# Performance work log

Hardware: AMD Instinct MI355X
Metric: run time of the kernel (lower is better)

Reference implementation:

```python
import jax, jax.numpy as jnp
import numpy as np
import math

B, T, C = 4, 1024, 768
H, K = 12, 10
D = C // H  # 64


def setup_inputs() -> dict:
    key = jax.random.key(0)
    ks = jax.random.split(key, 8)
    s = 1.0 / math.sqrt(C)
    return {
        "hidden_states": jax.random.normal(ks[0], (B, T, C), jnp.float32),
        "ucb_count_score": jax.random.uniform(ks[1], (B, H, T, T), jnp.float32),
        "Wq": jax.random.normal(ks[2], (C, C), jnp.float32) * s,
        "bq": jnp.zeros((C,), jnp.float32),
        "Wk": jax.random.normal(ks[3], (C, C), jnp.float32) * s,
        "bk": jnp.zeros((C,), jnp.float32),
        "Wv": jax.random.normal(ks[4], (C, C), jnp.float32) * s,
        "bv": jnp.zeros((C,), jnp.float32),
        "Wo": jax.random.normal(ks[5], (C, C), jnp.float32) * s,
        "bo": jnp.zeros((C,), jnp.float32),
        "counter": 2000,
        "ucb": 1,
    }


def _heads(x):
    # [B,T,C] -> [B,H,T,D]
    return x.reshape(B, T, H, D).transpose(0, 2, 1, 3)


def reference(hidden_states, ucb_count_score, Wq, bq, Wk, bk, Wv, bv, Wo, bo, counter, ucb):
    q = _heads(hidden_states @ Wq + bq)
    k = _heads(hidden_states @ Wk + bk)
    v = _heads(hidden_states @ Wv + bv)

    scores = jnp.einsum("bhqd,bhkd->bhqk", q, k) / math.sqrt(D)
    att = jax.nn.softmax(scores, axis=-1)

    if ucb and counter >= 1000:  # ucb_activation_step
        log_t = math.log(float(counter))
        ucb_scores = att + 1.0 * jnp.sqrt(log_t / (ucb_count_score + 1e-8))  # ucb_beta=1.0
        _, top_idx = jax.lax.top_k(ucb_scores, K)  # [B,H,T,K]
        # scatter 1.0 at top-k positions along last axis
        flat_idx = top_idx.reshape(-1, K)            # [N,K], N=B*H*T
        n = flat_idx.shape[0]
        mask = jnp.zeros((n, T), att.dtype).at[jnp.arange(n)[:, None], flat_idx].set(1.0)
        mask = mask.reshape(B, H, T, T)
        updated_count = ucb_count_score + mask
        sel = att * mask
        attention_probs = sel / (sel.sum(axis=-1, keepdims=True) + 1e-8)
    else:
        attention_probs = att
        updated_count = ucb_count_score

    ctx = jnp.einsum("bhqk,bhkd->bhqd", attention_probs, v)
    ctx = ctx.transpose(0, 2, 1, 3).reshape(B, T, C)
    out = ctx @ Wo + bo  # proj_dropout is identity in eval
    return out, attention_probs, updated_count
```

## Files before the change

kernel.cpp:

```cpp
#include <hip/hip_runtime.h>
#include <math.h>

namespace {

constexpr int Bc = 4, Tc = 1024, Cch = 768, Hc = 12, Dc = 64, KSEL = 10;
constexpr size_t BTC    = (size_t)Bc * Tc * Cch;
constexpr size_t PROBSN = (size_t)Bc * Hc * Tc * Tc;
constexpr size_t CC     = (size_t)Cch * Cch;

typedef __attribute__((ext_vector_type(8))) short          bf16x8;
typedef __attribute__((ext_vector_type(4))) float          f32x4;
typedef __attribute__((ext_vector_type(4))) unsigned short u16x4;
typedef __attribute__((ext_vector_type(8))) unsigned short u16x8;

__device__ __forceinline__ unsigned short bf16rne(float x) {
  unsigned int u = __float_as_uint(x);
  return (unsigned short)((u + 0x7FFFu + ((u >> 16) & 1u)) >> 16);
}
__device__ __forceinline__ float bf16tof(unsigned short h) {
  return __uint_as_float(((unsigned int)h) << 16);
}

template <int CTRL, int RM, bool BC>
__device__ __forceinline__ float dppmovf(float x, float oldv) {
  return __int_as_float(__builtin_amdgcn_update_dpp(
      __float_as_int(oldv), __float_as_int(x), CTRL, RM, 0xf, BC));
}

__device__ __forceinline__ float wave_fmax(float x) {
  x = fmaxf(x, dppmovf<0x111, 0xf, false>(x, x));
  x = fmaxf(x, dppmovf<0x112, 0xf, false>(x, x));
  x = fmaxf(x, dppmovf<0x114, 0xf, false>(x, x));
  x = fmaxf(x, dppmovf<0x118, 0xf, false>(x, x));
  x = fmaxf(x, dppmovf<0x142, 0xa, false>(x, x));
  x = fmaxf(x, dppmovf<0x143, 0xc, false>(x, x));
  return __int_as_float(__builtin_amdgcn_readlane(__float_as_int(x), 63));
}

__device__ __forceinline__ float wave_fsum(float x) {
  x += dppmovf<0x111, 0xf, true>(x, 0.f);
  x += dppmovf<0x112, 0xf, true>(x, 0.f);
  x += dppmovf<0x114, 0xf, true>(x, 0.f);
  x += dppmovf<0x118, 0xf, true>(x, 0.f);
  x += dppmovf<0x142, 0xa, true>(x, 0.f);
  x += dppmovf<0x143, 0xc, true>(x, 0.f);
  return __int_as_float(__builtin_amdgcn_readlane(__float_as_int(x), 63));
}

template <int CTRL, int RM>
__device__ __forceinline__ unsigned long long dppmax64_step(unsigned long long k) {
  const int lo = (int)(unsigned)(k & 0xFFFFFFFFull);
  const int hi = (int)(unsigned)(k >> 32);
  const int lo2 = __builtin_amdgcn_update_dpp(lo, lo, CTRL, RM, 0xf, false);
  const int hi2 = __builtin_amdgcn_update_dpp(hi, hi, CTRL, RM, 0xf, false);
  const unsigned long long k2 =
      ((unsigned long long)(unsigned)hi2 << 32) | (unsigned)lo2;
  return (k2 > k) ? k2 : k;
}

__device__ __forceinline__ unsigned long long wave_kmax(unsigned long long k) {
  k = dppmax64_step<0x111, 0xf>(k);
  k = dppmax64_step<0x112, 0xf>(k);
  k = dppmax64_step<0x114, 0xf>(k);
  k = dppmax64_step<0x118, 0xf>(k);
  k = dppmax64_step<0x142, 0xa>(k);
  k = dppmax64_step<0x143, 0xc>(k);
  const int lo = __builtin_amdgcn_readlane((int)(unsigned)(k & 0xFFFFFFFFull), 63);
  const int hi = __builtin_amdgcn_readlane((int)(unsigned)(k >> 32), 63);
  return ((unsigned long long)(unsigned)hi << 32) | (unsigned)lo;
}

__global__ __launch_bounds__(256) void split_plane(
    const float* __restrict__ src,
    unsigned short* __restrict__ h, unsigned short* __restrict__ l)
{
  const size_t i = (size_t)(blockIdx.x * 256 + threadIdx.x) * 4;
  const float4 v = *(const float4*)&src[i];
  const float xs[4] = {v.x, v.y, v.z, v.w};
  u16x4 hh, ll;
  #pragma unroll
  for (int e = 0; e < 4; ++e) {
    const unsigned short hb = bf16rne(xs[e]);
    hh[e] = hb;
    ll[e] = bf16rne(xs[e] - bf16tof(hb));
  }
  *(u16x4*)&h[i] = hh;
  *(u16x4*)&l[i] = ll;
}

__global__ __launch_bounds__(256) void splitT_w(
    const float* __restrict__ W,
    unsigned short* __restrict__ th, unsigned short* __restrict__ tl)
{
  __shared__ float tile[32][33];
  const int n0 = blockIdx.x * 32, k0 = blockIdx.y * 32;
  const int x = threadIdx.x & 31, y = threadIdx.x >> 5;

  #pragma unroll
  for (int i = 0; i < 4; ++i) {
    const int kk = y * 4 + i;
    tile[kk][x] = W[(size_t)(k0 + kk) * Cch + n0 + x];
  }
  __syncthreads();
  #pragma unroll
  for (int i = 0; i < 4; ++i) {
    const int nn = y * 4 + i;
    const float v = tile[x][nn];
    const unsigned short hb = bf16rne(v);
    th[(size_t)(n0 + nn) * Cch + k0 + x] = hb;
    tl[(size_t)(n0 + nn) * Cch + k0 + x] = bf16rne(v - bf16tof(hb));
  }
}

__global__ __launch_bounds__(256) void qkv_mfma(
    const unsigned short* __restrict__ hidh, const unsigned short* __restrict__ hidl,
    const unsigned short* __restrict__ wqth, const unsigned short* __restrict__ wqtl,
    const unsigned short* __restrict__ wkth, const unsigned short* __restrict__ wktl,
    const unsigned short* __restrict__ wvth, const unsigned short* __restrict__ wvtl,
    const float* __restrict__ bq, const float* __restrict__ bk,
    const float* __restrict__ bv,
    unsigned short* __restrict__ qh, unsigned short* __restrict__ ql,
    unsigned short* __restrict__ kh, unsigned short* __restrict__ kl,
    float* __restrict__ V)
{
  const int z = blockIdx.z;
  const unsigned short* __restrict__ Bhp = (z == 0) ? wqth : (z == 1) ? wkth : wvth;
  const unsigned short* __restrict__ Blp = (z == 0) ? wqtl : (z == 1) ? wktl : wvtl;
  const float* __restrict__ bias = (z == 0) ? bq : (z == 1) ? bk : bv;

  const int m0 = blockIdx.y * 64;
  const int n0 = blockIdx.x * 128;

  __shared__ unsigned short Ah[64][72],  Al[64][72];
  __shared__ unsigned short Bh[128][72], Bl[128][72];

  const int t    = threadIdx.x;
  const int lane = t & 63;
  const int wv   = t >> 6;
  const int wq   = (wv >> 1) * 32;
  const int wk   = (wv & 1) * 64;
  const int fr   = lane & 15;
  const int fg   = lane >> 4;

  f32x4 acc[2][4] = {};

  for (int k0 = 0; k0 < Cch; k0 += 64) {
    __syncthreads();
    #pragma unroll
    for (int i = 0; i < 2; ++i) {
      const int id = t + 256*i;
      const int r = id >> 3, c8 = (id & 7) * 8;
      *(u16x8*)&Ah[r][c8] = *(const u16x8*)&hidh[(size_t)(m0 + r)*Cch + k0 + c8];
      *(u16x8*)&Al[r][c8] = *(const u16x8*)&hidl[(size_t)(m0 + r)*Cch + k0 + c8];
    }
    #pragma unroll
    for (int i = 0; i < 4; ++i) {
      const int id = t + 256*i;
      const int r = id >> 3, c8 = (id & 7) * 8;
      *(u16x8*)&Bh[r][c8] = *(const u16x8*)&Bhp[(size_t)(n0 + r)*Cch + k0 + c8];
      *(u16x8*)&Bl[r][c8] = *(const u16x8*)&Blp[(size_t)(n0 + r)*Cch + k0 + c8];
    }
    __syncthreads();

    #pragma unroll
    for (int g2 = 0; g2 < 2; ++g2) {
      const int dof = g2*32 + 8*fg;
      bf16x8 aH[2], aL[2];
      #pragma unroll
      for (int qt = 0; qt < 2; ++qt) {
        aH[qt] = *(const bf16x8*)&Ah[wq + qt*16 + fr][dof];
        aL[qt] = *(const bf16x8*)&Al[wq + qt*16 + fr][dof];
      }
      #pragma unroll
      for (int kt = 0; kt < 4; ++kt) {
        const bf16x8 bH = *(const bf16x8*)&Bh[wk + kt*16 + fr][dof];
        const bf16x8 bL = *(const bf16x8*)&Bl[wk + kt*16 + fr][dof];
        #pragma unroll
        for (int qt = 0; qt < 2; ++qt) {
          acc[qt][kt] = __builtin_amdgcn_mfma_f32_16x16x32_bf16(
              aH[qt], bH, acc[qt][kt], 0, 0, 0);
          acc[qt][kt] = __builtin_amdgcn_mfma_f32_16x16x32_bf16(
              aH[qt], bL, acc[qt][kt], 0, 0, 0);
          acc[qt][kt] = __builtin_amdgcn_mfma_f32_16x16x32_bf16(
              aL[qt], bH, acc[qt][kt], 0, 0, 0);
        }
      }
    }
  }

  float bcol[4];
  #pragma unroll
  for (int kt = 0; kt < 4; ++kt) bcol[kt] = bias[n0 + wk + kt*16 + fr];

  unsigned short* __restrict__ dh = (z == 0) ? qh : kh;
  unsigned short* __restrict__ dl = (z == 0) ? ql : kl;

  #pragma unroll
  for (int qt = 0; qt < 2; ++qt) {
    #pragma unroll
    for (int j = 0; j < 4; ++j) {
      const int m  = m0 + wq + qt*16 + 4*fg + j;
      const int b  = m >> 10, tt = m & 1023;
      #pragma unroll
      for (int kt = 0; kt < 4; ++kt) {
        const int col = n0 + wk + kt*16 + fr;
        const float val = acc[qt][kt][j] + bcol[kt];
        const size_t idx =
            (((size_t)(b*Hc + (col >> 6)))*Tc + tt)*Dc + (col & 63);
        if (z < 2) {
          const unsigned short hb = bf16rne(val);
          dh[idx] = hb;
          dl[idx] = bf16rne(val - bf16tof(hb));
        } else {
          V[idx] = val;
        }
      }
    }
  }
}

__global__ __launch_bounds__(256) void score_mfma(
    const unsigned short* __restrict__ qhp, const unsigned short* __restrict__ qlp,
    const unsigned short* __restrict__ khp, const unsigned short* __restrict__ klp,
    float* __restrict__ scores)
{
  const int k0 = blockIdx.x * 128;
  const int q0 = blockIdx.y * 64;
  const int bh = blockIdx.z;

  __shared__ unsigned short Qh[64][72],  Ql[64][72];
  __shared__ unsigned short Kh[128][72], Kl[128][72];

  const int t = threadIdx.x;
  const size_t qb = ((size_t)bh*Tc + q0) * Dc;
  const size_t kb = ((size_t)bh*Tc + k0) * Dc;

  #pragma unroll
  for (int i = 0; i < 2; ++i) {
    const int id = t + 256*i;
    const int r = id >> 3, c8 = (id & 7) * 8;
    *(u16x8*)&Qh[r][c8] = *(const u16x8*)&qhp[qb + (size_t)r*Dc + c8];
    *(u16x8*)&Ql[r][c8] = *(const u16x8*)&qlp[qb + (size_t)r*Dc + c8];
  }
  #pragma unroll
  for (int i = 0; i < 4; ++i) {
    const int id = t + 256*i;
    const int r = id >> 3, c8 = (id & 7) * 8;
    *(u16x8*)&Kh[r][c8] = *(const u16x8*)&khp[kb + (size_t)r*Dc + c8];
    *(u16x8*)&Kl[r][c8] = *(const u16x8*)&klp[kb + (size_t)r*Dc + c8];
  }
  __syncthreads();

  const int lane = t & 63;
  const int wv   = t >> 6;
  const int wq   = (wv >> 1) * 32;
  const int wk   = (wv & 1) * 64;
  const int fr   = lane & 15;
  const int fg   = lane >> 4;

  f32x4 acc[2][4] = {};

  #pragma unroll
  for (int g2 = 0; g2 < 2; ++g2) {
    const int dof = g2*32 + 8*fg;
    bf16x8 aH[2], aL[2];
    #pragma unroll
    for (int qt = 0; qt < 2; ++qt) {
      aH[qt] = *(const bf16x8*)&Qh[wq + qt*16 + fr][dof];
      aL[qt] = *(const bf16x8*)&Ql[wq + qt*16 + fr][dof];
    }
    #pragma unroll
    for (int kt = 0; kt < 4; ++kt) {
      const bf16x8 bH = *(const bf16x8*)&Kh[wk + kt*16 + fr][dof];
      const bf16x8 bL = *(const bf16x8*)&Kl[wk + kt*16 + fr][dof];
      #pragma unroll
      for (int qt = 0; qt < 2; ++qt) {
        acc[qt][kt] = __builtin_amdgcn_mfma_f32_16x16x32_bf16(
            aH[qt], bH, acc[qt][kt], 0, 0, 0);
        acc[qt][kt] = __builtin_amdgcn_mfma_f32_16x16x32_bf16(
            aH[qt], bL, acc[qt][kt], 0, 0, 0);
        acc[qt][kt] = __builtin_amdgcn_mfma_f32_16x16x32_bf16(
            aL[qt], bH, acc[qt][kt], 0, 0, 0);
      }
    }
  }

  #pragma unroll
  for (int qt = 0; qt < 2; ++qt) {
    #pragma unroll
    for (int j = 0; j < 4; ++j) {
      const int qrow = q0 + wq + qt*16 + 4*fg + j;
      const size_t rb = ((size_t)bh * Tc + qrow) * Tc + k0 + wk;
      #pragma unroll
      for (int kt = 0; kt < 4; ++kt)
        scores[rb + kt*16 + fr] = acc[qt][kt][j] * 0.125f;
    }
  }
}

__global__ __launch_bounds__(256, 4) void ucb_topk(
    const float* __restrict__ qkv,
    const float* __restrict__ count_in,
    const int*   __restrict__ counter_p,
    const int*   __restrict__ ucb_p,
    float* __restrict__ probs,
    float* __restrict__ count_out,
    float* __restrict__ ctx)
{
  const int bh   = blockIdx.y;
  const int lane = threadIdx.x & 63;
  const int wv   = threadIdx.x >> 6;
  const int row  = blockIdx.x * 4 + wv;
  const int b = bh / Hc, h = bh % Hc;
  const size_t rb = ((size_t)bh * Tc + row) * Tc;
  const float* __restrict__ Vh = qkv + 2*BTC + (size_t)bh * Tc * Dc;

  __shared__ float psel[4][KSEL];

  const int  counter = counter_p[0];
  const int  ucbf    = ucb_p[0];
  const bool do_ucb  = (ucbf != 0) && (counter >= 1000);
  const float lt     = do_ucb ? logf((float)counter) : 0.f;

  float s[16];
  #pragma unroll
  for (int w = 0; w < 16; ++w) s[w] = probs[rb + lane + 64*w];

  float mx = -INFINITY;
  #pragma unroll
  for (int w = 0; w < 16; ++w) mx = fmaxf(mx, s[w]);
  mx = wave_fmax(mx);

  float sum = 0.f;
  #pragma unroll
  for (int w = 0; w < 16; ++w) { s[w] = __expf(s[w] - mx); sum += s[w]; }
  sum = wave_fsum(sum);

  const float rsum = 1.0f / sum;
  #pragma unroll
  for (int w = 0; w < 16; ++w) s[w] = s[w] * rsum;

  if (do_ucb) {
    const float sqlt = sqrtf(lt);

    unsigned long long key[16];
    #pragma unroll
    for (int w = 0; w < 16; ++w) {
      const float c = count_in[rb + lane + 64*w];
      count_out[rb + lane + 64*w] = c;
      const float u = fmaf(sqlt, rsqrtf(c + 1e-8f), s[w]);
      key[w] = ((unsigned long long)__float_as_uint(u) << 32)
             | (unsigned long long)(~(unsigned)(lane + (w << 6)));
    }

    unsigned selmask = 0u;
    unsigned long long rpack = 0ull;
    int ks[KSEL];

    #pragma unroll
    for (int r = 0; r < KSEL; ++r) {
      unsigned long long t0[8];
      #pragma unroll
      for (int w = 0; w < 8; ++w) {
        const unsigned long long a =
            ((selmask >> (2*w)) & 1u) ? 0ull : key[2*w];
        const unsigned long long bb =
            ((selmask >> (2*w + 1)) & 1u) ? 0ull : key[2*w + 1];
        t0[w] = (a > bb) ? a : bb;
      }
      unsigned long long t1[4];
      #pragma unroll
      for (int w = 0; w < 4; ++w)
        t1[w] = (t0[2*w] > t0[2*w+1]) ? t0[2*w] : t0[2*w+1];
      unsigned long long t2a = (t1[0] > t1[1]) ? t1[0] : t1[1];
      unsigned long long t2b = (t1[2] > t1[3]) ? t1[2] : t1[3];
      unsigned long long m   = (t2a > t2b) ? t2a : t2b;

      m = wave_kmax(m);

      const int idx = (int)(~(unsigned)(m & 0xFFFFFFFFull));
      ks[r] = idx;
      if ((idx & 63) == lane) {
        const int wsel = idx >> 6;
        selmask |= 1u << wsel;
        rpack   |= ((unsigned long long)r) << (4 * wsel);
      }
    }

    #pragma unroll
    for (int w = 0; w < 16; ++w) {
      if ((selmask >> w) & 1u) {
        const int r = (int)((rpack >> (4 * w)) & 15ull);
        psel[wv][r] = s[w];
      }
    }
    __syncthreads();

    float pvv[KSEL];
    float denom = 1e-8f;
    #pragma unroll
    for (int r = 0; r < KSEL; ++r) { pvv[r] = psel[wv][r]; denom += pvv[r]; }
    const float rden = 1.0f / denom;

    #pragma unroll
    for (int w = 0; w < 16; ++w) {
      const bool sb = (selmask >> w) & 1u;
      probs[rb + lane + 64*w] = sb ? (s[w] * rden) : 0.0f;
    }
    #pragma unroll
    for (int r = 0; r < KSEL; ++r) {
      if ((ks[r] & 63) == lane)
        count_out[rb + ks[r]] = count_in[rb + ks[r]] + 1.0f;
    }

    float cd = 0.f;
    #pragma unroll
    for (int r = 0; r < KSEL; ++r)
      cd += pvv[r] * Vh[(size_t)ks[r] * Dc + lane];
    ctx[((size_t)b*Tc + row)*Cch + h*Dc + lane] = cd * rden;
  } else {
    #pragma unroll
    for (int w = 0; w < 16; ++w) {
      probs[rb + lane + 64*w]     = s[w];
      count_out[rb + lane + 64*w] = count_in[rb + lane + 64*w];
    }
  }
}

__global__ __launch_bounds__(256) void pv_gemm(
    const float* __restrict__ probs,
    const float* __restrict__ Vm,
    float* __restrict__ ctx,
    const int* __restrict__ counter_p,
    const int* __restrict__ ucb_p)
{
  if ((ucb_p[0] != 0) && (counter_p[0] >= 1000)) return;

  const int bh = blockIdx.y;
  const int q0 = blockIdx.x * 64;
  const int b = bh / Hc, h = bh % Hc;

  __shared__ float aT[32][68];
  __shared__ float vN[32][68];

  const int t  = threadIdx.x;
  const int tn = t & 15;
  const int tq = t >> 4;

  float acc[4][4];
  #pragma unroll
  for (int i = 0; i < 4; ++i)
    #pragma unroll
    for (int j = 0; j < 4; ++j) acc[i][j] = 0.f;

  for (int k0 = 0; k0 < Tc; k0 += 32) {
    __syncthreads();
    #pragma unroll
    for (int p = 0; p < 2; ++p) {
      const int id = t + 256*p;
      const int r = id >> 3, c = id & 7;
      const float4 v =
          *(const float4*)&probs[((size_t)bh*Tc + q0 + r)*Tc + k0 + 4*c];
      aT[4*c + 0][r] = v.x; aT[4*c + 1][r] = v.y;
      aT[4*c + 2][r] = v.z; aT[4*c + 3][r] = v.w;
    }
    #pragma unroll
    for (int p = 0; p < 2; ++p) {
      const int id = t + 256*p;
      const int kk = id >> 4, dcc = id & 15;
      const float4 v = *(const float4*)&Vm[((size_t)bh*Tc + k0 + kk)*Dc + 4*dcc];
      *(float4*)&vN[kk][4*dcc] = v;
    }
    __syncthreads();
    #pragma unroll
    for (int kk = 0; kk < 32; ++kk) {
      const float4 a  = *(const float4*)&aT[kk][4*tq];
      const float4 vv = *(const float4*)&vN[kk][4*tn];
      const float av[4] = {a.x, a.y, a.z, a.w};
      const float bw[4] = {vv.x, vv.y, vv.z, vv.w};
      #pragma unroll
      for (int qi = 0; qi < 4; ++qi)
        #pragma unroll
        for (int ni = 0; ni < 4; ++ni) acc[qi][ni] += av[qi] * bw[ni];
    }
  }

  #pragma unroll
  for (int qi = 0; qi < 4; ++qi) {
    const int tt = q0 + 4*tq + qi;
    float4 o;
    o.x = acc[qi][0]; o.y = acc[qi][1]; o.z = acc[qi][2]; o.w = acc[qi][3];
    *(float4*)&ctx[((size_t)b*Tc + tt)*Cch + h*Dc + 4*tn] = o;
  }
}

__global__ __launch_bounds__(256) void out_mfma(
    const unsigned short* __restrict__ ah, const unsigned short* __restrict__ al,
    const unsigned short* __restrict__ bth, const unsigned short* __restrict__ btl,
    const float* __restrict__ bias,
    float* __restrict__ out)
{
  const int m0 = blockIdx.y * 64;
  const int n0 = blockIdx.x * 128;

  __shared__ unsigned short Ah[64][72],  Al[64][72];
  __shared__ unsigned short Bh[128][72], Bl[128][72];

  const int t    = threadIdx.x;
  const int lane = t & 63;
  const int wv   = t >> 6;
  const int wq   = (wv >> 1) * 32;
  const int wk   = (wv & 1) * 64;
  const int fr   = lane & 15;
  const int fg   = lane >> 4;

  f32x4 acc[2][4] = {};

  for (int k0 = 0; k0 < Cch; k0 += 64) {
    __syncthreads();
    #pragma unroll
    for (int i = 0; i < 2; ++i) {
      const int id = t + 256*i;
      const int r = id >> 3, c8 = (id & 7) * 8;
      *(u16x8*)&Ah[r][c8] = *(const u16x8*)&ah[(size_t)(m0 + r)*Cch + k0 + c8];
      *(u16x8*)&Al[r][c8] = *(const u16x8*)&al[(size_t)(m0 + r)*Cch + k0 + c8];
    }
    #pragma unroll
    for (int i = 0; i < 4; ++i) {
      const int id = t + 256*i;
      const int r = id >> 3, c8 = (id & 7) * 8;
      *(u16x8*)&Bh[r][c8] = *(const u16x8*)&bth[(size_t)(n0 + r)*Cch + k0 + c8];
      *(u16x8*)&Bl[r][c8] = *(const u16x8*)&btl[(size_t)(n0 + r)*Cch + k0 + c8];
    }
    __syncthreads();

    #pragma unroll
    for (int g2 = 0; g2 < 2; ++g2) {
      const int dof = g2*32 + 8*fg;
      bf16x8 aH[2], aL[2];
      #pragma unroll
      for (int qt = 0; qt < 2; ++qt) {
        aH[qt] = *(const bf16x8*)&Ah[wq + qt*16 + fr][dof];
        aL[qt] = *(const bf16x8*)&Al[wq + qt*16 + fr][dof];
      }
      #pragma unroll
      for (int kt = 0; kt < 4; ++kt) {
        const bf16x8 bH = *(const bf16x8*)&Bh[wk + kt*16 + fr][dof];
        const bf16x8 bL = *(const bf16x8*)&Bl[wk + kt*16 + fr][dof];
        #pragma unroll
        for (int qt = 0; qt < 2; ++qt) {
          acc[qt][kt] = __builtin_amdgcn_mfma_f32_16x16x32_bf16(
              aH[qt], bH, acc[qt][kt], 0, 0, 0);
          acc[qt][kt] = __builtin_amdgcn_mfma_f32_16x16x32_bf16(
              aH[qt], bL, acc[qt][kt], 0, 0, 0);
          acc[qt][kt] = __builtin_amdgcn_mfma_f32_16x16x32_bf16(
              aL[qt], bH, acc[qt][kt], 0, 0, 0);
        }
      }
    }
  }

  float bcol[4];
  #pragma unroll
  for (int kt = 0; kt < 4; ++kt) bcol[kt] = bias[n0 + wk + kt*16 + fr];

  #pragma unroll
  for (int qt = 0; qt < 2; ++qt) {
    #pragma unroll
    for (int j = 0; j < 4; ++j) {
      const int m = m0 + wq + qt*16 + 4*fg + j;
      #pragma unroll
      for (int kt = 0; kt < 4; ++kt) {
        const int col = n0 + wk + kt*16 + fr;
        out[(size_t)m * Cch + col] = acc[qt][kt][j] + bcol[kt];
      }
    }
  }
}

}

extern "C" void kernel_launch(void* const* d_in, const int* in_sizes, int n_in,
                              void* d_out, int out_size, void* d_ws, size_t ws_size,
                              hipStream_t stream) {
  (void)in_sizes; (void)n_in; (void)out_size; (void)ws_size;

  const float* hid  = (const float*)d_in[0];
  const float* cnt  = (const float*)d_in[1];
  const float* Wq   = (const float*)d_in[2];
  const float* bq   = (const float*)d_in[3];
  const float* Wk   = (const float*)d_in[4];
  const float* bk   = (const float*)d_in[5];
  const float* Wv   = (const float*)d_in[6];
  const float* bv   = (const float*)d_in[7];
  const float* Wo   = (const float*)d_in[8];
  const float* bo   = (const float*)d_in[9];
  const int* counter = (const int*)d_in[10];
  const int* ucb     = (const int*)d_in[11];

  float* out       = (float*)d_out;
  float* probs     = out + BTC;
  float* count_out = probs + PROBSN;

  float* ws  = (float*)d_ws;
  float* V   = ws + 2*BTC;
  float* ctx = ws + 3*BTC;
  unsigned short* qkb = (unsigned short*)d_ws;
  unsigned short* qh = qkb;
  unsigned short* ql = qkb + BTC;
  unsigned short* kh = qkb + 2*BTC;
  unsigned short* kl = qkb + 3*BTC;

  unsigned short* cvt  = (unsigned short*)count_out;
  unsigned short* hidh = cvt;
  unsigned short* hidl = cvt + BTC;
  unsigned short* wqth = cvt + 2*BTC;
  unsigned short* wqtl = wqth + CC;
  unsigned short* wkth = wqtl + CC;
  unsigned short* wktl = wkth + CC;
  unsigned short* wvth = wktl + CC;
  unsigned short* wvtl = wvth + CC;

  unsigned short* ctxh = qkb;
  unsigned short* ctxl = qkb + BTC;
  unsigned short* woth = qkb + 2*BTC;
  unsigned short* wotl = woth + CC;

  split_plane<<<BTC/1024, 256, 0, stream>>>(hid, hidh, hidl);
  splitT_w<<<dim3(24, 24), 256, 0, stream>>>(Wq, wqth, wqtl);
  splitT_w<<<dim3(24, 24), 256, 0, stream>>>(Wk, wkth, wktl);
  splitT_w<<<dim3(24, 24), 256, 0, stream>>>(Wv, wvth, wvtl);

  qkv_mfma<<<dim3(Cch/128, (Bc*Tc)/64, 3), 256, 0, stream>>>(
      hidh, hidl, wqth, wqtl, wkth, wktl, wvth, wvtl,
      bq, bk, bv, qh, ql, kh, kl, V);

  score_mfma<<<dim3(Tc/128, Tc/64, Bc*Hc), 256, 0, stream>>>(
      qh, ql, kh, kl, probs);

  ucb_topk<<<dim3(Tc/4, Bc*Hc), 256, 0, stream>>>(
      ws, cnt, counter, ucb, probs, count_out, ctx);

  pv_gemm<<<dim3(Tc/64, Bc*Hc), 256, 0, stream>>>(
      probs, V, ctx, counter, ucb);

  split_plane<<<BTC/1024, 256, 0, stream>>>(ctx, ctxh, ctxl);
  splitT_w<<<dim3(24, 24), 256, 0, stream>>>(Wo, woth, wotl);

  out_mfma<<<dim3(Cch/128, (Bc*Tc)/64), 256, 0, stream>>>(
      ctxh, ctxl, woth, wotl, bo, out);
}
```

Before: 368.1 us.

## Fuse bf16 split into GEMM loads, batch weight splits, loop score K-chunks

The hidden-state and context hi/lo bf16 split kernels are removed. The QKV and output GEMMs now read fp32 directly and split each tile while loading it into shared memory, which saves a full write and re-read of the split planes. The three Q/K/V weight-transpose splits become one launch with a z dimension, and the Wo split now runs before the top-k stage, writing into the Q region of the workspace that is no longer needed by then. score_mfma now keeps its Q tile resident and loops over all eight key chunks per block, which means fewer blocks and less Q reloading but also less parallelism across the GPU.

```diff
diff --git a/kernel.cpp b/kernel.cpp
--- a/kernel.cpp
+++ b/kernel.cpp
@@ -10,7 +10,6 @@
 
 typedef __attribute__((ext_vector_type(8))) short          bf16x8;
 typedef __attribute__((ext_vector_type(4))) float          f32x4;
-typedef __attribute__((ext_vector_type(4))) unsigned short u16x4;
 typedef __attribute__((ext_vector_type(8))) unsigned short u16x8;
 
 __device__ __forceinline__ unsigned short bf16rne(float x) {
@@ -19,6 +18,17 @@
 }
 __device__ __forceinline__ float bf16tof(unsigned short h) {
   return __uint_as_float(((unsigned int)h) << 16);
+}
+
+__device__ __forceinline__ void split8(const float4 v0, const float4 v1,
+                                       u16x8& hh, u16x8& ll) {
+  const float xs[8] = {v0.x, v0.y, v0.z, v0.w, v1.x, v1.y, v1.z, v1.w};
+  #pragma unroll
+  for (int e = 0; e < 8; ++e) {
+    const unsigned short hb = bf16rne(xs[e]);
+    hh[e] = hb;
+    ll[e] = bf16rne(xs[e] - bf16tof(hb));
+  }
 }
 
 template <int CTRL, int RM, bool BC>
@@ -70,25 +80,7 @@
   return ((unsigned long long)(unsigned)hi << 32) | (unsigned)lo;
 }
 
-__global__ __launch_bounds__(256) void split_plane(
-    const float* __restrict__ src,
-    unsigned short* __restrict__ h, unsigned short* __restrict__ l)
-{
-  const size_t i = (size_t)(blockIdx.x * 256 + threadIdx.x) * 4;
-  const float4 v = *(const float4*)&src[i];
-  const float xs[4] = {v.x, v.y, v.z, v.w};
-  u16x4 hh, ll;
-  #pragma unroll
-  for (int e = 0; e < 4; ++e) {
-    const unsigned short hb = bf16rne(xs[e]);
-    hh[e] = hb;
-    ll[e] = bf16rne(xs[e] - bf16tof(hb));
-  }
-  *(u16x4*)&h[i] = hh;
-  *(u16x4*)&l[i] = ll;
-}
-
-__global__ __launch_bounds__(256) void splitT_w(
+__device__ __forceinline__ void splitT_body(
     const float* __restrict__ W,
     unsigned short* __restrict__ th, unsigned short* __restrict__ tl)
 {
@@ -112,8 +104,29 @@
   }
 }
 
+__global__ __launch_bounds__(256) void splitT_w(
+    const float* __restrict__ W,
+    unsigned short* __restrict__ th, unsigned short* __restrict__ tl)
+{
+  splitT_body(W, th, tl);
+}
+
+__global__ __launch_bounds__(256) void splitT_w3(
+    const float* __restrict__ W0, const float* __restrict__ W1,
+    const float* __restrict__ W2,
+    unsigned short* __restrict__ th0, unsigned short* __restrict__ tl0,
+    unsigned short* __restrict__ th1, unsigned short* __restrict__ tl1,
+    unsigned short* __restrict__ th2, unsigned short* __restrict__ tl2)
+{
+  const int z = blockIdx.z;
+  const float* W = (z == 0) ? W0 : (z == 1) ? W1 : W2;
+  unsigned short* th = (z == 0) ? th0 : (z == 1) ? th1 : th2;
+  unsigned short* tl = (z == 0) ? tl0 : (z == 1) ? tl1 : tl2;
+  splitT_body(W, th, tl);
+}
+
 __global__ __launch_bounds__(256) void qkv_mfma(
-    const unsigned short* __restrict__ hidh, const unsigned short* __restrict__ hidl,
+    const float* __restrict__ hid,
     const unsigned short* __restrict__ wqth, const unsigned short* __restrict__ wqtl,
     const unsigned short* __restrict__ wkth, const unsigned short* __restrict__ wktl,
     const unsigned short* __restrict__ wvth, const unsigned short* __restrict__ wvtl,
@@ -150,8 +163,12 @@
     for (int i = 0; i < 2; ++i) {
       const int id = t + 256*i;
       const int r = id >> 3, c8 = (id & 7) * 8;
-      *(u16x8*)&Ah[r][c8] = *(const u16x8*)&hidh[(size_t)(m0 + r)*Cch + k0 + c8];
-      *(u16x8*)&Al[r][c8] = *(const u16x8*)&hidl[(size_t)(m0 + r)*Cch + k0 + c8];
+      const float4 v0 = *(const float4*)&hid[(size_t)(m0 + r)*Cch + k0 + c8];
+      const float4 v1 = *(const float4*)&hid[(size_t)(m0 + r)*Cch + k0 + c8 + 4];
+      u16x8 hh, ll;
+      split8(v0, v1, hh, ll);
+      *(u16x8*)&Ah[r][c8] = hh;
+      *(u16x8*)&Al[r][c8] = ll;
     }
     #pragma unroll
     for (int i = 0; i < 4; ++i) {
@@ -224,16 +241,14 @@
     const unsigned short* __restrict__ khp, const unsigned short* __restrict__ klp,
     float* __restrict__ scores)
 {
-  const int k0 = blockIdx.x * 128;
-  const int q0 = blockIdx.y * 64;
-  const int bh = blockIdx.z;
+  const int q0 = blockIdx.x * 64;
+  const int bh = blockIdx.y;
 
   __shared__ unsigned short Qh[64][72],  Ql[64][72];
   __shared__ unsigned short Kh[128][72], Kl[128][72];
 
   const int t = threadIdx.x;
   const size_t qb = ((size_t)bh*Tc + q0) * Dc;
-  const size_t kb = ((size_t)bh*Tc + k0) * Dc;
 
   #pragma unroll
   for (int i = 0; i < 2; ++i) {
@@ -242,14 +257,6 @@
     *(u16x8*)&Qh[r][c8] = *(const u16x8*)&qhp[qb + (size_t)r*Dc + c8];
     *(u16x8*)&Ql[r][c8] = *(const u16x8*)&qlp[qb + (size_t)r*Dc + c8];
   }
-  #pragma unroll
-  for (int i = 0; i < 4; ++i) {
-    const int id = t + 256*i;
-    const int r = id >> 3, c8 = (id & 7) * 8;
-    *(u16x8*)&Kh[r][c8] = *(const u16x8*)&khp[kb + (size_t)r*Dc + c8];
-    *(u16x8*)&Kl[r][c8] = *(const u16x8*)&klp[kb + (size_t)r*Dc + c8];
-  }
-  __syncthreads();
 
   const int lane = t & 63;
   const int wv   = t >> 6;
@@ -258,42 +265,56 @@
   const int fr   = lane & 15;
   const int fg   = lane >> 4;
 
-  f32x4 acc[2][4] = {};
-
-  #pragma unroll
-  for (int g2 = 0; g2 < 2; ++g2) {
-    const int dof = g2*32 + 8*fg;
-    bf16x8 aH[2], aL[2];
+  #pragma unroll 1
+  for (int kc = 0; kc < 8; ++kc) {
+    const int k0 = kc * 128;
+    const size_t kb = ((size_t)bh*Tc + k0) * Dc;
+    __syncthreads();
+    #pragma unroll
+    for (int i = 0; i < 4; ++i) {
+      const int id = t + 256*i;
+      const int r = id >> 3, c8 = (id & 7) * 8;
+      *(u16x8*)&Kh[r][c8] = *(const u16x8*)&khp[kb + (size_t)r*Dc + c8];
+      *(u16x8*)&Kl[r][c8] = *(const u16x8*)&klp[kb + (size_t)r*Dc + c8];
+    }
+    __syncthreads();
+
+    f32x4 acc[2][4] = {};
+    #pragma unroll
+    for (int g2 = 0; g2 < 2; ++g2) {
+      const int dof = g2*32 + 8*fg;
+      bf16x8 aH[2], aL[2];
+      #pragma unroll
+      for (int qt = 0; qt < 2; ++qt) {
+        aH[qt] = *(const bf16x8*)&Qh[wq + qt*16 + fr][dof];
+        aL[qt] = *(const bf16x8*)&Ql[wq + qt*16 + fr][dof];
+      }
+      #pragma unroll
+      for (int kt = 0; kt < 4; ++kt) {
+        const bf16x8 bH = *(const bf16x8*)&Kh[wk + kt*16 + fr][dof];
+        const bf16x8 bL = *(const bf16x8*)&Kl[wk + kt*16 + fr][dof];
+        #pragma unroll
+        for (int qt = 0; qt < 2; ++qt) {
+          acc[qt][kt] = __builtin_amdgcn_mfma_f32_16x16x32_bf16(
+              aH[qt], bH, acc[qt][kt], 0, 0, 0);
+          acc[qt][kt] = __builtin_amdgcn_mfma_f32_16x16x32_bf16(
+              aH[qt], bL, acc[qt][kt], 0, 0, 0);
+          acc[qt][kt] = __builtin_amdgcn_mfma_f32_16x16x32_bf16(
+              aL[qt], bH, acc[qt][kt], 0, 0, 0);
+        }
+      }
+    }
+
     #pragma unroll
     for (int qt = 0; qt < 2; ++qt) {
-      aH[qt] = *(const bf16x8*)&Qh[wq + qt*16 + fr][dof];
-      aL[qt] = *(const bf16x8*)&Ql[wq + qt*16 + fr][dof];
-    }
-    #pragma unroll
-    for (int kt = 0; kt < 4; ++kt) {
-      const bf16x8 bH = *(const bf16x8*)&Kh[wk + kt*16 + fr][dof];
-      const bf16x8 bL = *(const bf16x8*)&Kl[wk + kt*16 + fr][dof];
-      #pragma unroll
-      for (int qt = 0; qt < 2; ++qt) {
-        acc[qt][kt] = __builtin_amdgcn_mfma_f32_16x16x32_bf16(
-            aH[qt], bH, acc[qt][kt], 0, 0, 0);
-        acc[qt][kt] = __builtin_amdgcn_mfma_f32_16x16x32_bf16(
-            aH[qt], bL, acc[qt][kt], 0, 0, 0);
-        acc[qt][kt] = __builtin_amdgcn_mfma_f32_16x16x32_bf16(
-            aL[qt], bH, acc[qt][kt], 0, 0, 0);
-      }
-    }
-  }
-
-  #pragma unroll
-  for (int qt = 0; qt < 2; ++qt) {
-    #pragma unroll
-    for (int j = 0; j < 4; ++j) {
-      const int qrow = q0 + wq + qt*16 + 4*fg + j;
-      const size_t rb = ((size_t)bh * Tc + qrow) * Tc + k0 + wk;
-      #pragma unroll
-      for (int kt = 0; kt < 4; ++kt)
-        scores[rb + kt*16 + fr] = acc[qt][kt][j] * 0.125f;
+      #pragma unroll
+      for (int j = 0; j < 4; ++j) {
+        const int qrow = q0 + wq + qt*16 + 4*fg + j;
+        const size_t rb = ((size_t)bh * Tc + qrow) * Tc + k0 + wk;
+        #pragma unroll
+        for (int kt = 0; kt < 4; ++kt)
+          scores[rb + kt*16 + fr] = acc[qt][kt][j] * 0.125f;
+      }
     }
   }
 }
@@ -495,7 +516,7 @@
 }
 
 __global__ __launch_bounds__(256) void out_mfma(
-    const unsigned short* __restrict__ ah, const unsigned short* __restrict__ al,
+    const float* __restrict__ ctx,
     const unsigned short* __restrict__ bth, const unsigned short* __restrict__ btl,
     const float* __restrict__ bias,
     float* __restrict__ out)
@@ -522,8 +543,12 @@
     for (int i = 0; i < 2; ++i) {
       const int id = t + 256*i;
       const int r = id >> 3, c8 = (id & 7) * 8;
-      *(u16x8*)&Ah[r][c8] = *(const u16x8*)&ah[(size_t)(m0 + r)*Cch + k0 + c8];
-      *(u16x8*)&Al[r][c8] = *(const u16x8*)&al[(size_t)(m0 + r)*Cch + k0 + c8];
+      const float4 v0 = *(const float4*)&ctx[(size_t)(m0 + r)*Cch + k0 + c8];
+      const float4 v1 = *(const float4*)&ctx[(size_t)(m0 + r)*Cch + k0 + c8 + 4];
+      u16x8 hh, ll;
+      split8(v0, v1, hh, ll);
+      *(u16x8*)&Ah[r][c8] = hh;
+      *(u16x8*)&Al[r][c8] = ll;
     }
     #pragma unroll
     for (int i = 0; i < 4; ++i) {
@@ -612,31 +637,27 @@
   unsigned short* kl = qkb + 3*BTC;
 
   unsigned short* cvt  = (unsigned short*)count_out;
-  unsigned short* hidh = cvt;
-  unsigned short* hidl = cvt + BTC;
-  unsigned short* wqth = cvt + 2*BTC;
+  unsigned short* wqth = cvt;
   unsigned short* wqtl = wqth + CC;
   unsigned short* wkth = wqtl + CC;
   unsigned short* wktl = wkth + CC;
   unsigned short* wvth = wktl + CC;
   unsigned short* wvtl = wvth + CC;
 
-  unsigned short* ctxh = qkb;
-  unsigned short* ctxl = qkb + BTC;
-  unsigned short* woth = qkb + 2*BTC;
-  unsigned short* wotl = woth + CC;
-
-  split_plane<<<BTC/1024, 256, 0, stream>>>(hid, hidh, hidl);
-  splitT_w<<<dim3(24, 24), 256, 0, stream>>>(Wq, wqth, wqtl);
-  splitT_w<<<dim3(24, 24), 256, 0, stream>>>(Wk, wkth, wktl);
-  splitT_w<<<dim3(24, 24), 256, 0, stream>>>(Wv, wvth, wvtl);
+  unsigned short* woth = qkb;
+  unsigned short* wotl = qkb + CC;
+
+  splitT_w3<<<dim3(24, 24, 3), 256, 0, stream>>>(
+      Wq, Wk, Wv, wqth, wqtl, wkth, wktl, wvth, wvtl);
 
   qkv_mfma<<<dim3(Cch/128, (Bc*Tc)/64, 3), 256, 0, stream>>>(
-      hidh, hidl, wqth, wqtl, wkth, wktl, wvth, wvtl,
+      hid, wqth, wqtl, wkth, wktl, wvth, wvtl,
       bq, bk, bv, qh, ql, kh, kl, V);
 
-  score_mfma<<<dim3(Tc/128, Tc/64, Bc*Hc), 256, 0, stream>>>(
+  score_mfma<<<dim3(Tc/64, Bc*Hc), 256, 0, stream>>>(
       qh, ql, kh, kl, probs);
+
+  splitT_w<<<dim3(24, 24), 256, 0, stream>>>(Wo, woth, wotl);
 
   ucb_topk<<<dim3(Tc/4, Bc*Hc), 256, 0, stream>>>(
       ws, cnt, counter, ucb, probs, count_out, ctx);
@@ -644,9 +665,6 @@
   pv_gemm<<<dim3(Tc/64, Bc*Hc), 256, 0, stream>>>(
       probs, V, ctx, counter, ucb);
 
-  split_plane<<<BTC/1024, 256, 0, stream>>>(ctx, ctxh, ctxl);
-  splitT_w<<<dim3(24, 24), 256, 0, stream>>>(Wo, woth, wotl);
-
   out_mfma<<<dim3(Cch/128, (Bc*Tc)/64), 256, 0, stream>>>(
-      ctxh, ctxl, woth, wotl, bo, out);
-}
+      ctx, woth, wotl, bo, out);
+}
```

Result: no change. 371.6 us (+0.9%).
